# Performance work log

Hardware: AMD Instinct MI355X
Metric: run time of the kernel (lower is better)

## Reference

```python
import jax, jax.numpy as jnp
import numpy as np

B, C, T = 8, 512, 2048
G = 32          # GroupNorm groups
HEADS = 8       # C // head_channels(64)
EPS = 1e-5


def setup_inputs() -> dict:
    key = jax.random.key(0)
    ks = jax.random.split(key, 7)
    s = 0.02
    return {
        "x": jax.random.normal(ks[0], (B, C, T), dtype=jnp.float32),
        "gn_w": jnp.ones((C,), dtype=jnp.float32),
        "gn_b": jnp.zeros((C,), dtype=jnp.float32),
        "qkv_w": jax.random.normal(ks[1], (3 * C, C), dtype=jnp.float32) * s,
        "qkv_b": jnp.zeros((3 * C,), dtype=jnp.float32),
        "proj_w": jax.random.normal(ks[2], (C, C), dtype=jnp.float32) * s,
        "proj_b": jnp.zeros((C,), dtype=jnp.float32),
    }


def reference(x, gn_w, gn_b, qkv_w, qkv_b, proj_w, proj_b):
    b, c, t = x.shape
    ch = c // HEADS
    # GroupNorm(32, C): normalize over (channels-in-group, T)
    xg = x.reshape(b, G, (c // G) * t)
    mu = jnp.mean(xg, axis=-1, keepdims=True)
    var = jnp.var(xg, axis=-1, keepdims=True)
    h = ((xg - mu) * jax.lax.rsqrt(var + EPS)).reshape(b, c, t)
    h = h * gn_w[:, None] + gn_b[:, None]
    # 1x1 Conv1d -> pointwise linear over channels
    qkv = jnp.einsum('oc,bct->bot', qkv_w, h) + qkv_b[:, None]  # [b, 3c, t]
    q, k, v = jnp.split(qkv, 3, axis=1)
    scale = ch ** -0.25
    q = (q * scale).reshape(b * HEADS, ch, t)
    k = (k * scale).reshape(b * HEADS, ch, t)
    v = v.reshape(b * HEADS, ch, t)
    w = jnp.einsum('bct,bcs->bts', q, k)  # [b*H, t, t]
    w = jax.nn.softmax(w.astype(jnp.float32), axis=-1).astype(q.dtype)
    a = jnp.einsum('bts,bcs->bct', w, v).reshape(b, c, t)
    out = jnp.einsum('oc,bct->bot', proj_w, a) + proj_b[:, None]
    return x + out
```

## Files before the change

### kernel.cpp

```cpp
#include <hip/hip_runtime.h>
#include <hip/hip_bf16.h>
#include <math.h>

#define NB 8
#define NC 512
#define NT 2048
#define NG 32
#define NH 8
#define CH 64

typedef __attribute__((ext_vector_type(8))) short short8;
typedef __attribute__((ext_vector_type(4))) short short4v;
typedef __attribute__((ext_vector_type(4))) float floatx4;
typedef __attribute__((ext_vector_type(2))) unsigned int uintx2;
typedef __attribute__((ext_vector_type(4))) unsigned int uintx4;

static __device__ __forceinline__ short f2bf(float f) {
    __hip_bfloat16 h = __float2bfloat16(f);
    return *reinterpret_cast<short*>(&h);
}

static __device__ __forceinline__ int pk2bf_trunc(float lo, float hi) {
    return (int)__builtin_amdgcn_perm(__builtin_bit_cast(unsigned, hi),
                                      __builtin_bit_cast(unsigned, lo),
                                      0x07060302u);
}

static __device__ __forceinline__ void gload_lds16(const short* g, short* l) {
    __builtin_amdgcn_global_load_lds(
        (const __attribute__((address_space(1))) void*)g,
        (__attribute__((address_space(3))) void*)l, 16, 0, 0);
}

__global__ __launch_bounds__(256) void castw_kernel(
    const float* __restrict__ qw, const float* __restrict__ pw,
    short* __restrict__ qo, short* __restrict__ po)
{
    const int i = blockIdx.x * 256 + threadIdx.x;
    const bool isq = i < 196608;
    const int j = isq ? i : i - 196608;
    float4 v = isq ? ((const float4*)qw)[j] : ((const float4*)pw)[j];
    short4v s;
    s.x = f2bf(v.x); s.y = f2bf(v.y); s.z = f2bf(v.z); s.w = f2bf(v.w);
    if (isq) *(short4v*)&qo[j * 4] = s;
    else     *(short4v*)&po[j * 4] = s;
}

__global__ __launch_bounds__(256) void gn_stats_kernel(
    const float* __restrict__ x, float* __restrict__ stats)
{
    __shared__ float red[16];
    const int tid = threadIdx.x;
    const int grp = blockIdx.x;
    const float4* xp = (const float4*)(x + (size_t)grp * 16 * NT);

    float s = 0.f, ss = 0.f;
    for (int i = tid; i < 8192; i += 256) {
        float4 v = xp[i];
        s  += v.x + v.y + v.z + v.w;
        ss += v.x*v.x + v.y*v.y + v.z*v.z + v.w*v.w;
    }
    #pragma unroll
    for (int o = 32; o > 0; o >>= 1) {
        s  += __shfl_down(s,  o, 64);
        ss += __shfl_down(ss, o, 64);
    }
    const int lane = tid & 63, wid = tid >> 6;
    if (lane == 0) { red[wid] = s; red[8 + wid] = ss; }
    __syncthreads();
    if (tid == 0) {
        const float inv = 1.f / 32768.f;
        const float mean = (red[0] + red[1] + red[2] + red[3]) * inv;
        const float var  = (red[8] + red[9] + red[10] + red[11]) * inv - mean * mean;
        stats[grp * 2]     = mean;
        stats[grp * 2 + 1] = rsqrtf(var + 1e-5f);
    }
}

__global__ __launch_bounds__(256) void gn_apply_kernel(
    const float* __restrict__ x, const float* __restrict__ gw,
    const float* __restrict__ gb, const float* __restrict__ stats,
    short* __restrict__ ht)
{
    __shared__ float wc_s[NC], bc_s[NC];
    __shared__ float tile[64 * 68];
    const int tid = threadIdx.x;
    const int b = blockIdx.y;
    const int t0 = blockIdx.x * 64;

    for (int c = tid; c < NC; c += 256) {
        const int g = c >> 4;
        const float mean = stats[(b * NG + g) * 2];
        const float rstd = stats[(b * NG + g) * 2 + 1];
        const float wc = gw[c] * rstd;
        wc_s[c] = wc;
        bc_s[c] = gb[c] - mean * wc;
    }

    const int cl = tid >> 2;
    const int k4 = tid & 3;
    const int tl = tid >> 2;
    const int cs = (tid & 3) * 16;

    for (int p = 0; p < 8; ++p) {
        const int c0 = p * 64;
        __syncthreads();
        const float* src = x + ((size_t)b * NC + c0 + cl) * NT + t0;
        #pragma unroll
        for (int k = 0; k < 4; ++k) {
            float4 v = *(const float4*)(src + k4 * 16 + k * 4);
            *(float4*)&tile[cl * 68 + k4 * 16 + k * 4] = v;
        }
        __syncthreads();
        short v16[16];
        #pragma unroll
        for (int j = 0; j < 16; ++j) {
            const int c = c0 + cs + j;
            v16[j] = f2bf(tile[(cs + j) * 68 + tl] * wc_s[c] + bc_s[c]);
        }
        short* dst = ht + ((size_t)b * NT + t0 + tl) * NC + c0 + cs;
        *(short8*)&dst[0] = *(const short8*)&v16[0];
        *(short8*)&dst[8] = *(const short8*)&v16[8];
    }
}

#define BK 32
__global__ __launch_bounds__(256) void qkv_gemm_kernel(
    const short* __restrict__ wb, const short* __restrict__ ht,
    const float* __restrict__ bias,
    short* __restrict__ q_t, short* __restrict__ k_t, short* __restrict__ vv)
{
    __shared__ short As[128 * BK];
    __shared__ short Bs[128 * BK];
    const int tid = threadIdx.x;
    const int wv = tid >> 6, lane = tid & 63;
    const int l16 = lane & 15, quad = lane >> 4;
    const int fblk = blockIdx.y * 128 + blockIdx.x;
    const int jx = fblk >> 3, xcd = fblk & 7;
    const int n0 = (xcd * 16 + jx / 12) * 128;
    const int m0 = (jx % 12) * 128;
    const int wm = wv & 1, wn = wv >> 1;

    floatx4 acc[4][4];
    #pragma unroll
    for (int i = 0; i < 4; ++i)
        #pragma unroll
        for (int j = 0; j < 4; ++j) acc[i][j] = (floatx4){0.f, 0.f, 0.f, 0.f};

    const short* gsrc = (wv < 2) ? wb : ht;
    const int rbase = (wv & 1) * 64;
    const int tile0 = (wv < 2) ? m0 : n0;
    short* lbuf = (wv < 2) ? As : Bs;
    const int lrow = lane >> 2;
    const int lcol = (lane & 3) * 8;

    for (int k0 = 0; k0 < 512; k0 += BK) {
        __syncthreads();
        #pragma unroll
        for (int ch = 0; ch < 4; ++ch) {
            const int row = rbase + ch * 16 + lrow;
            gload_lds16(gsrc + (size_t)(tile0 + row) * 512 + k0 + lcol,
                        lbuf + (rbase + ch * 16) * BK);
        }
        __syncthreads();

        short8 af[4], bfr[4];
        #pragma unroll
        for (int i = 0; i < 4; ++i) {
            af[i]  = *(const short8*)&As[(wm * 64 + i * 16 + l16) * BK + quad * 8];
            bfr[i] = *(const short8*)&Bs[(wn * 64 + i * 16 + l16) * BK + quad * 8];
        }
        #pragma unroll
        for (int i = 0; i < 4; ++i)
            #pragma unroll
            for (int j = 0; j < 4; ++j)
                acc[i][j] = __builtin_amdgcn_mfma_f32_16x16x32_bf16(
                    af[i], bfr[j], acc[i][j], 0, 0, 0);
    }

    const float kscale = 0.35355339059327373f;
    const float qscale = 0.35355339059327373f * 1.4426950408889634f;
    #pragma unroll
    for (int i = 0; i < 4; ++i) {
        const int o16 = m0 + wm * 64 + i * 16;
        const int sel = o16 >> 9;
        const int hh  = (o16 >> 6) & 7;
        const int c16 = o16 & 63;
        const float4 b4 = *(const float4*)&bias[o16 + quad * 4];
        const float sc = (sel == 0) ? qscale : kscale;
        #pragma unroll
        for (int j = 0; j < 4; ++j) {
            const int tg = n0 + wn * 64 + j * 16 + l16;
            const int b = tg >> 11, t = tg & 2047;
            floatx4 v = acc[i][j];
            v[0] += b4.x; v[1] += b4.y; v[2] += b4.z; v[3] += b4.w;
            if (sel < 2) {
                short4v s;
                s.x = f2bf(v[0] * sc); s.y = f2bf(v[1] * sc);
                s.z = f2bf(v[2] * sc); s.w = f2bf(v[3] * sc);
                short* dst = (sel == 0 ? q_t : k_t) +
                    (((size_t)(b * NH + hh) * NT + t) * CH + c16 + quad * 4);
                *(short4v*)dst = s;
            } else {
                short* dst = vv + ((size_t)(b * NH + hh) * CH + c16 + quad * 4) * NT + t;
                #pragma unroll
                for (int r = 0; r < 4; ++r) dst[(size_t)r * NT] = f2bf(v[r]);
            }
        }
    }
}

__global__ __launch_bounds__(512, 4) void attn_kernel(
    const short* __restrict__ qg, const short* __restrict__ kg,
    const short* __restrict__ vg, short* __restrict__ at)
{
    __shared__ short kt[2][64 * 64];
    __shared__ short vs[2][64 * 64];

    const int tid = threadIdx.x;
    const int wv = tid >> 6, lane = tid & 63;
    const int l16 = lane & 15, quad = lane >> 4;
    const int xr = l16 & 7;
    const int t0 = blockIdx.x * 256;
    const int bh = blockIdx.y;
    const int b = bh >> 3, hd = bh & 7;
    const short* qh = qg + (size_t)bh * NT * CH;
    const short* kh = kg + (size_t)bh * NT * CH;
    const short* vh = vg + (size_t)bh * CH * NT;

    {
        const int row = tid >> 3, cc = (tid & 7) ^ (row & 7);
        gload_lds16(kh + (size_t)row * CH + cc * 8, &kt[0][wv * 512]);
        gload_lds16(vh + (size_t)row * NT + cc * 8, &vs[0][wv * 512]);
    }

    short8 bq[2][2];
    #pragma unroll
    for (int qt = 0; qt < 2; ++qt) {
        const int row = t0 + wv * 32 + qt * 16 + l16;
        #pragma unroll
        for (int ks = 0; ks < 2; ++ks)
            bq[qt][ks] = *(const short8*)&qh[(size_t)row * CH + ks * 32 + quad * 8];
    }
    __syncthreads();

    floatx4 Oa[4][2];
    #pragma unroll
    for (int ct = 0; ct < 4; ++ct)
        #pragma unroll
        for (int qt = 0; qt < 2; ++qt) Oa[ct][qt] = (floatx4){0.f, 0.f, 0.f, 0.f};
    float l_part[2] = {0.f, 0.f};

    for (int it = 0; it < NT / 64; ++it) {
        __syncthreads();
        if (it + 1 < NT / 64) {
            const int s0n = (it + 1) * 64;
            const int row = tid >> 3, cc = (tid & 7) ^ (row & 7);
            gload_lds16(kh + (size_t)(s0n + row) * CH + cc * 8,
                        &kt[(it + 1) & 1][wv * 512]);
            gload_lds16(vh + (size_t)row * NT + s0n + cc * 8,
                        &vs[(it + 1) & 1][wv * 512]);
        }
        const short* kc = kt[it & 1];
        const short* vc = vs[it & 1];

        floatx4 sacc[4][2];
        #pragma unroll
        for (int nt = 0; nt < 4; ++nt)
            #pragma unroll
            for (int qt = 0; qt < 2; ++qt) sacc[nt][qt] = (floatx4){0.f, 0.f, 0.f, 0.f};
        __builtin_amdgcn_s_setprio(1);
        #pragma unroll
        for (int ks = 0; ks < 2; ++ks) {
            const int c = (quad | (ks << 2)) ^ xr;
            #pragma unroll
            for (int nt = 0; nt < 4; ++nt) {
                short8 ak = *(const short8*)&kc[(nt * 16 + l16) * 64 + c * 8];
                #pragma unroll
                for (int qt = 0; qt < 2; ++qt)
                    sacc[nt][qt] = __builtin_amdgcn_mfma_f32_16x16x32_bf16(
                        ak, bq[qt][ks], sacc[nt][qt], 0, 0, 0);
            }
        }
        __builtin_amdgcn_s_setprio(0);

        unsigned pk01[2][4], pk23[2][4];
        #pragma unroll
        for (int qt = 0; qt < 2; ++qt) {
            float sn[4];
            #pragma unroll
            for (int nt = 0; nt < 4; ++nt) {
                const float p0 = __builtin_amdgcn_exp2f(sacc[nt][qt][0]);
                const float p1 = __builtin_amdgcn_exp2f(sacc[nt][qt][1]);
                const float p2 = __builtin_amdgcn_exp2f(sacc[nt][qt][2]);
                const float p3 = __builtin_amdgcn_exp2f(sacc[nt][qt][3]);
                sn[nt] = (p0 + p1) + (p2 + p3);
                pk01[qt][nt] = (unsigned)pk2bf_trunc(p0, p1);
                pk23[qt][nt] = (unsigned)pk2bf_trunc(p2, p3);
            }
            l_part[qt] += (sn[0] + sn[1]) + (sn[2] + sn[3]);
        }

        #pragma unroll
        for (int ks = 0; ks < 2; ++ks) {
            short8 bp[2];
            #pragma unroll
            for (int qt = 0; qt < 2; ++qt) {
                uintx2 a = __builtin_amdgcn_permlane32_swap(
                    pk01[qt][2 * ks], pk01[qt][2 * ks + 1], false, false);
                uintx2 w02 = __builtin_amdgcn_permlane16_swap(a.x, a.y, false, false);
                uintx2 c2 = __builtin_amdgcn_permlane32_swap(
                    pk23[qt][2 * ks], pk23[qt][2 * ks + 1], false, false);
                uintx2 w13 = __builtin_amdgcn_permlane16_swap(c2.x, c2.y, false, false);
                uintx4 wi = (uintx4){w02.x, w13.x, w02.y, w13.y};
                bp[qt] = __builtin_bit_cast(short8, wi);
            }
            const int c = (quad | (ks << 2)) ^ xr;
            __builtin_amdgcn_s_setprio(1);
            #pragma unroll
            for (int ct = 0; ct < 4; ++ct) {
                short8 av = *(const short8*)&vc[(ct * 16 + l16) * 64 + c * 8];
                #pragma unroll
                for (int qt = 0; qt < 2; ++qt)
                    Oa[ct][qt] = __builtin_amdgcn_mfma_f32_16x16x32_bf16(
                        av, bp[qt], Oa[ct][qt], 0, 0, 0);
            }
            __builtin_amdgcn_s_setprio(0);
        }
    }

    #pragma unroll
    for (int qt = 0; qt < 2; ++qt) {
        float l = l_part[qt];
        l += __shfl_xor(l, 16, 64);
        l += __shfl_xor(l, 32, 64);
        const float rl = 1.f / l;
        const int t = t0 + wv * 32 + qt * 16 + l16;
        short* dst = at + ((size_t)b * NT + t) * NC + hd * CH;
        #pragma unroll
        for (int ct = 0; ct < 4; ++ct) {
            int2 s;
            s.x = pk2bf_trunc(Oa[ct][qt][0] * rl, Oa[ct][qt][1] * rl);
            s.y = pk2bf_trunc(Oa[ct][qt][2] * rl, Oa[ct][qt][3] * rl);
            *(int2*)&dst[ct * 16 + quad * 4] = s;
        }
    }
}

__global__ __launch_bounds__(256) void proj_gemm_kernel(
    const short* __restrict__ wb, const short* __restrict__ at,
    const float* __restrict__ bias, const float* __restrict__ xres,
    float* __restrict__ out)
{
    __shared__ short As[128 * BK];
    __shared__ short Bs[128 * BK];
    const int tid = threadIdx.x;
    const int wv = tid >> 6, lane = tid & 63;
    const int l16 = lane & 15, quad = lane >> 4;
    const int fblk = blockIdx.y * 128 + blockIdx.x;
    const int jx = fblk >> 3, xcd = fblk & 7;
    const int n0 = (xcd * 16 + (jx >> 2)) * 128;
    const int m0 = (jx & 3) * 128;
    const int wm = wv & 1, wn = wv >> 1;

    floatx4 acc[4][4];
    #pragma unroll
    for (int i = 0; i < 4; ++i)
        #pragma unroll
        for (int j = 0; j < 4; ++j) acc[i][j] = (floatx4){0.f, 0.f, 0.f, 0.f};

    const short* gsrc = (wv < 2) ? wb : at;
    const int rbase = (wv & 1) * 64;
    const int tile0 = (wv < 2) ? m0 : n0;
    short* lbuf = (wv < 2) ? As : Bs;
    const int lrow = lane >> 2;
    const int lcol = (lane & 3) * 8;

    for (int k0 = 0; k0 < 512; k0 += BK) {
        __syncthreads();
        #pragma unroll
        for (int ch = 0; ch < 4; ++ch) {
            const int row = rbase + ch * 16 + lrow;
            gload_lds16(gsrc + (size_t)(tile0 + row) * 512 + k0 + lcol,
                        lbuf + (rbase + ch * 16) * BK);
        }
        __syncthreads();

        short8 af[4], bfr[4];
        #pragma unroll
        for (int i = 0; i < 4; ++i) {
            af[i]  = *(const short8*)&As[(wm * 64 + i * 16 + l16) * BK + quad * 8];
            bfr[i] = *(const short8*)&Bs[(wn * 64 + i * 16 + l16) * BK + quad * 8];
        }
        #pragma unroll
        for (int i = 0; i < 4; ++i)
            #pragma unroll
            for (int j = 0; j < 4; ++j)
                acc[i][j] = __builtin_amdgcn_mfma_f32_16x16x32_bf16(
                    af[i], bfr[j], acc[i][j], 0, 0, 0);
    }

    #pragma unroll
    for (int i = 0; i < 4; ++i) {
        const int o16 = m0 + wm * 64 + i * 16;
        const float4 b4 = *(const float4*)&bias[o16 + quad * 4];
        #pragma unroll
        for (int j = 0; j < 4; ++j) {
            const int tg = n0 + wn * 64 + j * 16 + l16;
            const int b = tg >> 11, t = tg & 2047;
            const size_t base = ((size_t)b * NC + o16 + quad * 4) * NT + t;
            floatx4 v = acc[i][j];
            out[base]          = v[0] + b4.x + xres[base];
            out[base + NT]     = v[1] + b4.y + xres[base + NT];
            out[base + 2 * NT] = v[2] + b4.z + xres[base + 2 * NT];
            out[base + 3 * NT] = v[3] + b4.w + xres[base + 3 * NT];
        }
    }
}

extern "C" void kernel_launch(void* const* d_in, const int* in_sizes, int n_in,
                              void* d_out, int out_size, void* d_ws, size_t ws_size,
                              hipStream_t stream)
{
    const float* x      = (const float*)d_in[0];
    const float* gn_w   = (const float*)d_in[1];
    const float* gn_b   = (const float*)d_in[2];
    const float* qkv_w  = (const float*)d_in[3];
    const float* qkv_b  = (const float*)d_in[4];
    const float* proj_w = (const float*)d_in[5];
    const float* proj_b = (const float*)d_in[6];
    float* out = (float*)d_out;

    short* ht  = (short*)d_ws;
    short* q_t = ht  + 8388608;
    short* k_t = q_t + 8388608;
    short* vv  = k_t + 8388608;
    short* at  = vv  + 8388608;
    short* qwb = at  + 8388608;
    short* pwb = qwb + 786432;
    float* stats = (float*)(pwb + 262144);

    castw_kernel<<<1024, 256, 0, stream>>>(qkv_w, proj_w, qwb, pwb);
    gn_stats_kernel<<<NB * NG, 256, 0, stream>>>(x, stats);
    gn_apply_kernel<<<dim3(NT / 64, NB), 256, 0, stream>>>(x, gn_w, gn_b, stats, ht);
    qkv_gemm_kernel<<<dim3(128, 12), 256, 0, stream>>>(qwb, ht, qkv_b, q_t, k_t, vv);
    attn_kernel<<<dim3(NT / 256, NB * NH), 512, 0, stream>>>(q_t, k_t, vv, at);
    proj_gemm_kernel<<<dim3(128, 4), 256, 0, stream>>>(pwb, at, proj_b, x, out);
}
```

Before: 251.9 us.

## Fuse GroupNorm stats and apply into one LDS-resident kernel; remap attention blocks

Merges the GroupNorm statistics and apply kernels into one kernel. Each block loads a whole 16-channel group (128 KB) into LDS using direct global-to-LDS loads, reduces mean and variance there, then writes the normalized bf16 transposed output from LDS. This drops one launch, the stats buffer and the second read of x from global memory, but 128 KB of LDS per block limits occupancy to one block per CU, and only 256 blocks run. The attention grid is also remapped so that blocks sharing a time tile across heads are grouped by XCD, which is meant to improve L2 locality.

```diff
diff --git a/kernel.cpp b/kernel.cpp
--- a/kernel.cpp
+++ b/kernel.cpp
@@ -46,17 +46,31 @@
     else     *(short4v*)&po[j * 4] = s;
 }
 
-__global__ __launch_bounds__(256) void gn_stats_kernel(
-    const float* __restrict__ x, float* __restrict__ stats)
-{
+__global__ __launch_bounds__(256) void gn_fused_kernel(
+    const float* __restrict__ x, const float* __restrict__ gw,
+    const float* __restrict__ gb, short* __restrict__ ht)
+{
+    __shared__ float xs[16 * NT];
     __shared__ float red[16];
     const int tid = threadIdx.x;
-    const int grp = blockIdx.x;
-    const float4* xp = (const float4*)(x + (size_t)grp * 16 * NT);
+    const int wv = tid >> 6, lane = tid & 63;
+    const int f = blockIdx.x;
+    const int b = f & 7, g = f >> 3;
+
+    const float* src = x + ((size_t)b * NC + g * 16) * NT;
+
+    #pragma unroll
+    for (int i = 0; i < 32; ++i) {
+        const int slot = i * 256 + tid;
+        gload_lds16((const short*)src + (size_t)slot * 8,
+                    (short*)&xs[(i * 256 + wv * 64) * 4]);
+    }
+    __syncthreads();
 
     float s = 0.f, ss = 0.f;
-    for (int i = tid; i < 8192; i += 256) {
-        float4 v = xp[i];
+    #pragma unroll
+    for (int i = 0; i < 32; ++i) {
+        float4 v = ((const float4*)xs)[i * 256 + tid];
         s  += v.x + v.y + v.z + v.w;
         ss += v.x*v.x + v.y*v.y + v.z*v.z + v.w*v.w;
     }
@@ -65,62 +79,41 @@
         s  += __shfl_down(s,  o, 64);
         ss += __shfl_down(ss, o, 64);
     }
-    const int lane = tid & 63, wid = tid >> 6;
-    if (lane == 0) { red[wid] = s; red[8 + wid] = ss; }
+    if (lane == 0) { red[wv] = s; red[8 + wv] = ss; }
     __syncthreads();
-    if (tid == 0) {
-        const float inv = 1.f / 32768.f;
-        const float mean = (red[0] + red[1] + red[2] + red[3]) * inv;
-        const float var  = (red[8] + red[9] + red[10] + red[11]) * inv - mean * mean;
-        stats[grp * 2]     = mean;
-        stats[grp * 2 + 1] = rsqrtf(var + 1e-5f);
-    }
-}
-
-__global__ __launch_bounds__(256) void gn_apply_kernel(
-    const float* __restrict__ x, const float* __restrict__ gw,
-    const float* __restrict__ gb, const float* __restrict__ stats,
-    short* __restrict__ ht)
-{
-    __shared__ float wc_s[NC], bc_s[NC];
-    __shared__ float tile[64 * 68];
-    const int tid = threadIdx.x;
-    const int b = blockIdx.y;
-    const int t0 = blockIdx.x * 64;
-
-    for (int c = tid; c < NC; c += 256) {
-        const int g = c >> 4;
-        const float mean = stats[(b * NG + g) * 2];
-        const float rstd = stats[(b * NG + g) * 2 + 1];
-        const float wc = gw[c] * rstd;
-        wc_s[c] = wc;
-        bc_s[c] = gb[c] - mean * wc;
-    }
-
-    const int cl = tid >> 2;
-    const int k4 = tid & 3;
-    const int tl = tid >> 2;
-    const int cs = (tid & 3) * 16;
-
-    for (int p = 0; p < 8; ++p) {
-        const int c0 = p * 64;
-        __syncthreads();
-        const float* src = x + ((size_t)b * NC + c0 + cl) * NT + t0;
-        #pragma unroll
-        for (int k = 0; k < 4; ++k) {
-            float4 v = *(const float4*)(src + k4 * 16 + k * 4);
-            *(float4*)&tile[cl * 68 + k4 * 16 + k * 4] = v;
-        }
-        __syncthreads();
-        short v16[16];
-        #pragma unroll
-        for (int j = 0; j < 16; ++j) {
-            const int c = c0 + cs + j;
-            v16[j] = f2bf(tile[(cs + j) * 68 + tl] * wc_s[c] + bc_s[c]);
-        }
-        short* dst = ht + ((size_t)b * NT + t0 + tl) * NC + c0 + cs;
-        *(short8*)&dst[0] = *(const short8*)&v16[0];
-        *(short8*)&dst[8] = *(const short8*)&v16[8];
+    const float inv  = 1.f / 32768.f;
+    const float mean = (red[0] + red[1] + red[2] + red[3]) * inv;
+    const float var  = (red[8] + red[9] + red[10] + red[11]) * inv - mean * mean;
+    const float rstd = rsqrtf(var + 1e-5f);
+
+    float wc[16], bc[16];
+    #pragma unroll
+    for (int ch = 0; ch < 16; ++ch) {
+        const float w = gw[g * 16 + ch] * rstd;
+        wc[ch] = w;
+        bc[ch] = gb[g * 16 + ch] - mean * w;
+    }
+
+    #pragma unroll
+    for (int k = 0; k < 2; ++k) {
+        const int q = k * 256 + tid;
+        float4 col[16];
+        #pragma unroll
+        for (int ch = 0; ch < 16; ++ch)
+            col[ch] = *(const float4*)&xs[ch * NT + q * 4];
+        short* dst = ht + ((size_t)b * NT + q * 4) * NC + g * 16;
+        #pragma unroll
+        for (int j = 0; j < 4; ++j) {
+            short v16[16];
+            #pragma unroll
+            for (int ch = 0; ch < 16; ++ch) {
+                const float xv = (j == 0) ? col[ch].x : (j == 1) ? col[ch].y
+                               : (j == 2) ? col[ch].z : col[ch].w;
+                v16[ch] = f2bf(xv * wc[ch] + bc[ch]);
+            }
+            *(short8*)&dst[(size_t)j * NC]     = *(const short8*)&v16[0];
+            *(short8*)&dst[(size_t)j * NC + 8] = *(const short8*)&v16[8];
+        }
     }
 }
 
@@ -221,8 +214,9 @@
     const int wv = tid >> 6, lane = tid & 63;
     const int l16 = lane & 15, quad = lane >> 4;
     const int xr = l16 & 7;
-    const int t0 = blockIdx.x * 256;
-    const int bh = blockIdx.y;
+    const int f = blockIdx.y * 8 + blockIdx.x;
+    const int t0 = (f >> 6) * 256;
+    const int bh = ((f >> 3) & 7) * 8 + (f & 7);
     const int b = bh >> 3, hd = bh & 7;
     const short* qh = qg + (size_t)bh * NT * CH;
     const short* kh = kg + (size_t)bh * NT * CH;
@@ -438,11 +432,9 @@
     short* at  = vv  + 8388608;
     short* qwb = at  + 8388608;
     short* pwb = qwb + 786432;
-    float* stats = (float*)(pwb + 262144);
 
     castw_kernel<<<1024, 256, 0, stream>>>(qkv_w, proj_w, qwb, pwb);
-    gn_stats_kernel<<<NB * NG, 256, 0, stream>>>(x, stats);
-    gn_apply_kernel<<<dim3(NT / 64, NB), 256, 0, stream>>>(x, gn_w, gn_b, stats, ht);
+    gn_fused_kernel<<<NB * NG, 256, 0, stream>>>(x, gn_w, gn_b, ht);
     qkv_gemm_kernel<<<dim3(128, 12), 256, 0, stream>>>(qwb, ht, qkv_b, q_t, k_t, vv);
     attn_kernel<<<dim3(NT / 256, NB * NH), 512, 0, stream>>>(q_t, k_t, vv, at);
     proj_gemm_kernel<<<dim3(128, 4), 256, 0, stream>>>(pwb, at, proj_b, x, out);
```

New measurement: 229.8 us. 8.8% less time.
